# Kernel optimization log

Hardware: AMD Instinct MI355X
Metric: run time of the kernel (lower is better)

## Reference

```python
import jax, jax.numpy as jnp
import numpy as np

B, L = 1024, 256
D = 64        # neighbor_interaction_feat_dim
TD = 100      # time_encoder.dim
NUM_NODES = 20000


def setup_inputs() -> dict:
    key = jax.random.key(0)
    ks = jax.random.split(key, 12)
    return {
        "src_ids": jax.random.randint(ks[0], (B, L), 0, NUM_NODES),
        "dst_ids": jax.random.randint(ks[1], (B, L), 0, NUM_NODES),
        "src_times": jax.random.uniform(ks[2], (B, L), jnp.float32),
        "dst_times": jax.random.uniform(ks[3], (B, L), jnp.float32),
        "node_times": jax.random.uniform(ks[4], (B,), jnp.float32) + 1.0,
        "num_nodes": NUM_NODES,
        # LTF time encoder: cos(t * w + b)
        "w_time": jax.random.normal(ks[5], (TD,), jnp.float32),
        "b_time": jax.random.normal(ks[6], (TD,), jnp.float32) * 0.1,
        # time_to_scalar: Linear(TD, 1)
        "w_ts": jax.random.normal(ks[7], (TD,), jnp.float32) / np.sqrt(TD),
        "b_ts": jnp.zeros((), jnp.float32),
        # MLP: Linear(1, D) -> ReLU -> Linear(D, D)
        "w1": jax.random.normal(ks[8], (D,), jnp.float32),
        "b1": jax.random.normal(ks[9], (D,), jnp.float32) * 0.1,
        "w2": jax.random.normal(ks[10], (D, D), jnp.float32) / np.sqrt(D),
        "b2": jax.random.normal(ks[11], (D,), jnp.float32) * 0.1,
    }


def _histogram(ids, num_nodes):
    # per-row count of each node id, with id==0 treated as padding (count 0)
    b = ids.shape[0]
    mask = (ids != 0).astype(jnp.float32)
    hist = jnp.zeros((b, num_nodes), jnp.float32)
    return hist.at[jnp.arange(b)[:, None], ids].add(mask)


def _time_weight(time_diff, w_time, b_time, w_ts, b_ts):
    # LTF: cos(t*w + b) -> Linear(TD,1) -> sigmoid, all fused elementwise+dot
    feat = jnp.cos(time_diff[..., None] * w_time + b_time)  # (B,L,TD)
    return jax.nn.sigmoid(feat @ w_ts + b_ts)               # (B,L)


def _mlp_sum(weighted_counts, w1, b1, w2, b2):
    # weighted_counts: (B,L,2) scalar counts -> Linear(1,D) -> ReLU -> Linear(D,D), sum over axis 2
    h = jax.nn.relu(weighted_counts[..., None] * w1 + b1)   # (B,L,2,D)
    return (h @ w2 + b2).sum(axis=2)                        # (B,L,D)


def reference(src_ids, dst_ids, src_times, dst_times, node_times, num_nodes,
              w_time, b_time, w_ts, b_ts, w1, b1, w2, b2):
    hist_src = _histogram(src_ids, num_nodes)  # (B,N)
    hist_dst = _histogram(dst_ids, num_nodes)

    c_ss = jnp.take_along_axis(hist_src, src_ids, axis=1)
    c_sd = jnp.take_along_axis(hist_dst, src_ids, axis=1)
    c_ds = jnp.take_along_axis(hist_src, dst_ids, axis=1)
    c_dd = jnp.take_along_axis(hist_dst, dst_ids, axis=1)

    src_counts = jnp.stack([c_ss, c_sd], axis=2)  # (B,L,2)
    dst_counts = jnp.stack([c_ds, c_dd], axis=2)

    src_w = _time_weight(node_times[:, None] - src_times, w_time, b_time, w_ts, b_ts)
    dst_w = _time_weight(node_times[:, None] - dst_times, w_time, b_time, w_ts, b_ts)

    src_features = _mlp_sum(src_counts * src_w[..., None], w1, b1, w2, b2)
    dst_features = _mlp_sum(dst_counts * dst_w[..., None], w1, b1, w2, b2)
    return src_features, dst_features
```

## Files before the change

### kernel.cpp

```cpp
#include <hip/hip_runtime.h>

#define BB 1024
#define LL 256
#define DD 64
#define TDIM 100
#define NNODES 20000
#define HWORDS ((NNODES + 1) / 2)

typedef _Float16 half8_t __attribute__((ext_vector_type(8)));
typedef float f32x4 __attribute__((ext_vector_type(4)));

__global__ __launch_bounds__(256, 2) void tni_kernel(
    const int* __restrict__ src_ids, const int* __restrict__ dst_ids,
    const float* __restrict__ src_tm, const float* __restrict__ dst_tm,
    const float* __restrict__ node_tm,
    const float* __restrict__ w_time, const float* __restrict__ b_time,
    const float* __restrict__ w_ts, const float* __restrict__ b_ts,
    const float* __restrict__ w1, const float* __restrict__ b1,
    const float* __restrict__ w2, const float* __restrict__ b2,
    float* __restrict__ out)
{
    __shared__ unsigned int uS[10240];
    __shared__ float wrv[TDIM], brv[TDIM], wtsv[TDIM];
    __shared__ float w1v[DD], b1v[DD];

    unsigned int* hist = uS;
    half8_t* W2v = (half8_t*)uS;
    half8_t* Gv  = (half8_t*)(uS + 2048);

    const int t    = threadIdx.x;
    const int b    = blockIdx.x >> 1;
    const int side = blockIdx.x & 1;

    const int   sid   = src_ids[b*LL + t];
    const int   did   = dst_ids[b*LL + t];
    const float my_tm = side ? dst_tm[b*LL + t] : src_tm[b*LL + t];

    float w2r[16];
    #pragma unroll
    for (int i = 0; i < 16; ++i) w2r[i] = w2[t + 256*i];

    if (t < TDIM) {
        const float inv2pi = 0.15915494309189535f;
        wrv[t]  = w_time[t] * inv2pi;
        brv[t]  = b_time[t] * inv2pi;
        wtsv[t] = w_ts[t];
    }
    if (t < DD) {
        w1v[t] = w1[t];
        b1v[t] = b1[t];
    }

    const int sw = sid >> 1, ssh = (sid & 1) * 16;
    const int dw = did >> 1, dsh = (did & 1) * 16;
    const int myw  = side ? dw  : sw;
    const int mysh = side ? dsh : ssh;
    const int my_id = side ? did : sid;

    hist[sw] = 0; hist[dw] = 0;
    __syncthreads();
    if (sid) atomicAdd(&hist[sw], 1u << ssh);
    __syncthreads();
    unsigned c1 = (hist[myw] >> mysh) & 0xffffu;
    __syncthreads();
    hist[sw] = 0; hist[dw] = 0;
    __syncthreads();
    if (did) atomicAdd(&hist[dw], 1u << dsh);
    __syncthreads();
    unsigned c2 = (hist[myw] >> mysh) & 0xffffu;
    if (my_id == 0) { c1 = 0; c2 = 0; }
    __syncthreads();

    float td = node_tm[b] - my_tm;
    float z  = b_ts[0];
    #pragma unroll 4
    for (int k = 0; k < TDIM; ++k) {
        float r = fmaf(td, wrv[k], brv[k]);
        r -= floorf(r);
        z = fmaf(__builtin_amdgcn_cosf(r), wtsv[k], z);
    }
    float ee  = __builtin_amdgcn_exp2f(-1.44269504f * z);
    float wgt = __builtin_amdgcn_rcpf(1.0f + ee);
    float c1w = (float)c1 * wgt;
    float c2w = (float)c2 * wgt;

    {
        _Float16* w2s = (_Float16*)W2v;
        #pragma unroll
        for (int i = 0; i < 16; ++i) {
            int idx = t + 256*i;
            int e = idx >> 6, d = idx & 63;
            int chunk = (e >> 3) ^ (d & 7);
            w2s[d*64 + (chunk << 3) + (e & 7)] = (_Float16)w2r[i];
        }
    }

    #pragma unroll
    for (int c = 0; c < 8; ++c) {
        half8_t h;
        #pragma unroll
        for (int j = 0; j < 8; ++j) {
            float w1e = w1v[c*8 + j], b1e = b1v[c*8 + j];
            float g = fmaxf(fmaf(c1w, w1e, b1e), 0.f)
                    + fmaxf(fmaf(c2w, w1e, b1e), 0.f);
            h[j] = (_Float16)g;
        }
        Gv[t*8 + (c ^ (t & 7))] = h;
    }
    __syncthreads();

    const int w    = t >> 6;
    const int l    = t & 63;
    const int quad = l >> 4;
    const int lr   = l & 15;

    f32x4 acc[4][4];
    #pragma unroll
    for (int mt = 0; mt < 4; ++mt)
        #pragma unroll
        for (int nt = 0; nt < 4; ++nt) {
            f32x4 zz = {0.f, 0.f, 0.f, 0.f};
            acc[mt][nt] = zz;
        }

    #pragma unroll
    for (int s = 0; s < 2; ++s) {
        const int c = s*4 + quad;
        half8_t bfr[4], afr[4];
        #pragma unroll
        for (int nt = 0; nt < 4; ++nt) {
            int n = nt*16 + lr;
            bfr[nt] = W2v[n*8 + (c ^ (n & 7))];
        }
        #pragma unroll
        for (int mt = 0; mt < 4; ++mt) {
            int row = w*64 + mt*16 + lr;
            afr[mt] = Gv[row*8 + (c ^ (row & 7))];
        }
        #pragma unroll
        for (int mt = 0; mt < 4; ++mt)
            #pragma unroll
            for (int nt = 0; nt < 4; ++nt)
                acc[mt][nt] = __builtin_amdgcn_mfma_f32_16x16x32_f16(
                    afr[mt], bfr[nt], acc[mt][nt], 0, 0, 0);
    }

    float b2v[4];
    #pragma unroll
    for (int nt = 0; nt < 4; ++nt)
        b2v[nt] = 2.f * b2[nt*16 + lr];

    const int obase = side * (BB*LL*DD) + b * (LL*DD);
    #pragma unroll
    for (int mt = 0; mt < 4; ++mt) {
        #pragma unroll
        for (int r = 0; r < 4; ++r) {
            int pos = w*64 + mt*16 + quad*4 + r;
            #pragma unroll
            for (int nt = 0; nt < 4; ++nt) {
                out[obase + pos*DD + nt*16 + lr] = acc[mt][nt][r] + b2v[nt];
            }
        }
    }
}

extern "C" void kernel_launch(void* const* d_in, const int* in_sizes, int n_in,
                              void* d_out, int out_size, void* d_ws, size_t ws_size,
                              hipStream_t stream) {
    const int* src_ids = (const int*)d_in[0];
    const int* dst_ids = (const int*)d_in[1];
    const float* src_tm  = (const float*)d_in[2];
    const float* dst_tm  = (const float*)d_in[3];
    const float* node_tm = (const float*)d_in[4];
    const float* w_time = (const float*)d_in[6];
    const float* b_time = (const float*)d_in[7];
    const float* w_ts   = (const float*)d_in[8];
    const float* b_ts   = (const float*)d_in[9];
    const float* w1     = (const float*)d_in[10];
    const float* b1     = (const float*)d_in[11];
    const float* w2     = (const float*)d_in[12];
    const float* b2     = (const float*)d_in[13];
    float* out = (float*)d_out;

    tni_kernel<<<dim3(BB*2), dim3(256), 0, stream>>>(
        src_ids, dst_ids, src_tm, dst_tm, node_tm,
        w_time, b_time, w_ts, b_ts, w1, b1, w2, b2, out);
}
```

Before: 168.5 us.

## Merge src and dst sides into one 512-thread block per batch row

Each block now handles both the src and dst sides of one batch row with 512 threads, so every id is loaded and every histogram built once instead of redundantly by two blocks. The w2 staging is split across twice as many threads, and the output index is computed per row to pick the side. The range reduction also switches from floor-subtract to the hardware fract builtin. Shared memory use grows to about 74KB per block, which may limit blocks per CU despite the raised launch bounds.

Result: no change. 169.6 us (+0.7%).

```diff
diff --git a/kernel.cpp b/kernel.cpp
--- a/kernel.cpp
+++ b/kernel.cpp
@@ -5,12 +5,11 @@
 #define DD 64
 #define TDIM 100
 #define NNODES 20000
-#define HWORDS ((NNODES + 1) / 2)
 
 typedef _Float16 half8_t __attribute__((ext_vector_type(8)));
 typedef float f32x4 __attribute__((ext_vector_type(4)));
 
-__global__ __launch_bounds__(256, 2) void tni_kernel(
+__global__ __launch_bounds__(512, 4) void tni_kernel(
     const int* __restrict__ src_ids, const int* __restrict__ dst_ids,
     const float* __restrict__ src_tm, const float* __restrict__ dst_tm,
     const float* __restrict__ node_tm,
@@ -20,7 +19,7 @@
     const float* __restrict__ w2, const float* __restrict__ b2,
     float* __restrict__ out)
 {
-    __shared__ unsigned int uS[10240];
+    __shared__ unsigned int uS[18432];
     __shared__ float wrv[TDIM], brv[TDIM], wtsv[TDIM];
     __shared__ float w1v[DD], b1v[DD];
 
@@ -29,16 +28,16 @@
     half8_t* Gv  = (half8_t*)(uS + 2048);
 
     const int t    = threadIdx.x;
-    const int b    = blockIdx.x >> 1;
-    const int side = blockIdx.x & 1;
+    const int side = t >> 8;
+    const int pos  = t & 255;
+    const int b    = blockIdx.x;
 
-    const int   sid   = src_ids[b*LL + t];
-    const int   did   = dst_ids[b*LL + t];
-    const float my_tm = side ? dst_tm[b*LL + t] : src_tm[b*LL + t];
+    const int   my_id = side ? dst_ids[b*LL + pos] : src_ids[b*LL + pos];
+    const float my_tm = side ? dst_tm [b*LL + pos] : src_tm [b*LL + pos];
 
-    float w2r[16];
+    float w2r[8];
     #pragma unroll
-    for (int i = 0; i < 16; ++i) w2r[i] = w2[t + 256*i];
+    for (int i = 0; i < 8; ++i) w2r[i] = w2[t + 512*i];
 
     if (t < TDIM) {
         const float inv2pi = 0.15915494309189535f;
@@ -46,26 +45,23 @@
         brv[t]  = b_time[t] * inv2pi;
         wtsv[t] = w_ts[t];
     }
-    if (t < DD) {
-        w1v[t] = w1[t];
-        b1v[t] = b1[t];
+    else if (t >= 128 && t < 128 + DD) {
+        w1v[t-128] = w1[t-128];
+        b1v[t-128] = b1[t-128];
     }
 
-    const int sw = sid >> 1, ssh = (sid & 1) * 16;
-    const int dw = did >> 1, dsh = (did & 1) * 16;
-    const int myw  = side ? dw  : sw;
-    const int mysh = side ? dsh : ssh;
-    const int my_id = side ? did : sid;
+    const int myw  = my_id >> 1;
+    const int mysh = (my_id & 1) * 16;
 
-    hist[sw] = 0; hist[dw] = 0;
+    hist[myw] = 0;
     __syncthreads();
-    if (sid) atomicAdd(&hist[sw], 1u << ssh);
+    if (!side && my_id) atomicAdd(&hist[myw], 1u << mysh);
     __syncthreads();
     unsigned c1 = (hist[myw] >> mysh) & 0xffffu;
     __syncthreads();
-    hist[sw] = 0; hist[dw] = 0;
+    hist[myw] = 0;
     __syncthreads();
-    if (did) atomicAdd(&hist[dw], 1u << dsh);
+    if (side && my_id) atomicAdd(&hist[myw], 1u << mysh);
     __syncthreads();
     unsigned c2 = (hist[myw] >> mysh) & 0xffffu;
     if (my_id == 0) { c1 = 0; c2 = 0; }
@@ -75,8 +71,7 @@
     float z  = b_ts[0];
     #pragma unroll 4
     for (int k = 0; k < TDIM; ++k) {
-        float r = fmaf(td, wrv[k], brv[k]);
-        r -= floorf(r);
+        float r = __builtin_amdgcn_fractf(fmaf(td, wrv[k], brv[k]));
         z = fmaf(__builtin_amdgcn_cosf(r), wtsv[k], z);
     }
     float ee  = __builtin_amdgcn_exp2f(-1.44269504f * z);
@@ -87,8 +82,8 @@
     {
         _Float16* w2s = (_Float16*)W2v;
         #pragma unroll
-        for (int i = 0; i < 16; ++i) {
-            int idx = t + 256*i;
+        for (int i = 0; i < 8; ++i) {
+            int idx = t + 512*i;
             int e = idx >> 6, d = idx & 63;
             int chunk = (e >> 3) ^ (d & 7);
             w2s[d*64 + (chunk << 3) + (e & 7)] = (_Float16)w2r[i];
@@ -150,15 +145,17 @@
     for (int nt = 0; nt < 4; ++nt)
         b2v[nt] = 2.f * b2[nt*16 + lr];
 
-    const int obase = side * (BB*LL*DD) + b * (LL*DD);
+    const size_t halfo = (size_t)BB * LL * DD;
     #pragma unroll
     for (int mt = 0; mt < 4; ++mt) {
         #pragma unroll
         for (int r = 0; r < 4; ++r) {
-            int pos = w*64 + mt*16 + quad*4 + r;
+            int q = w*64 + mt*16 + quad*4 + r;
+            int qs = q >> 8, qp = q & 255;
             #pragma unroll
             for (int nt = 0; nt < 4; ++nt) {
-                out[obase + pos*DD + nt*16 + lr] = acc[mt][nt][r] + b2v[nt];
+                out[(size_t)qs*halfo + (size_t)b*(LL*DD) + qp*DD + nt*16 + lr] =
+                    acc[mt][nt][r] + b2v[nt];
             }
         }
     }
@@ -182,7 +179,7 @@
     const float* b2     = (const float*)d_in[13];
     float* out = (float*)d_out;
 
-    tni_kernel<<<dim3(BB*2), dim3(256), 0, stream>>>(
+    tni_kernel<<<dim3(BB), dim3(512), 0, stream>>>(
         src_ids, dst_ids, src_tm, dst_tm, node_tm,
         w_time, b_time, w_ts, b_ts, w1, b1, w2, b2, out);
 }
```
